# Optimization experiments

Measured on AMD Instinct MI355X. Metric: run time of the kernel, lower is better.

Reference implementation:

```python
import jax, jax.numpy as jnp
import numpy as np

N_NODES = 50000
N_EDGES = 1600000
IN_FEAT = 128
OUT_FEAT = 128
NUM_RELS = 8


def setup_inputs() -> dict:
    key = jax.random.key(0)
    k1, k2, k3, k4, k5, k6, k7 = jax.random.split(key, 7)
    x = jax.random.normal(k1, (N_NODES, IN_FEAT), dtype=jnp.float32)
    norm = jax.random.uniform(k2, (N_EDGES, 1), dtype=jnp.float32)
    src = jax.random.randint(k3, (N_EDGES,), 0, N_NODES)
    dst = jax.random.randint(k4, (N_EDGES,), 0, N_NODES)
    rel_type = jax.random.randint(k5, (N_EDGES,), 0, NUM_RELS)
    # Xavier-uniform-like init for the relation weight tensor (gain for relu)
    gain = float(np.sqrt(2.0))
    bound = gain * float(np.sqrt(6.0 / (IN_FEAT + OUT_FEAT)))
    weight = jax.random.uniform(k6, (NUM_RELS, IN_FEAT, OUT_FEAT), dtype=jnp.float32,
                                minval=-bound, maxval=bound)
    bias = jax.random.uniform(k7, (OUT_FEAT,), dtype=jnp.float32, minval=-0.1, maxval=0.1)
    return {"x": x, "norm": norm, "weight": weight, "bias": bias,
            "src": src, "dst": dst, "rel_type": rel_type}


def reference(x, norm, weight, bias, src, dst, rel_type):
    n_nodes = x.shape[0]
    # Transform every node feature by every relation matrix: [R, N, O].
    # This is equivalent math to the per-edge bmm(h_src, W[rel]) but avoids
    # materializing an [E, in, out] gathered weight tensor.
    hw = jnp.einsum('ni,rio->rno', x, weight)
    # Per-edge message: gather transformed src feature for edge's relation, scale by norm.
    msg = hw[rel_type, src] * norm            # [E, O]
    # Scatter-sum messages to destination nodes.
    h = jax.ops.segment_sum(msg, dst, num_segments=n_nodes)  # [N, O]
    h = jax.nn.relu(h + bias)
    return h
```

## Files before the change

kernel.cpp:

```cpp
#include <hip/hip_runtime.h>
#include <hip/hip_bf16.h>

typedef unsigned short u16;
typedef unsigned int u32;
typedef u16 u16x4 __attribute__((ext_vector_type(4)));
typedef u16 u16x8 __attribute__((ext_vector_type(8)));
typedef short bf16x8 __attribute__((ext_vector_type(8)));
typedef float f32x4 __attribute__((ext_vector_type(4)));

static __device__ __forceinline__ u16 f32_to_bf16(float f) {
    u32 b = __float_as_uint(f);
    u32 r = (b + 0x7fffu + ((b >> 16) & 1u)) >> 16;
    return (u16)r;
}
static __device__ __forceinline__ float bflo(u32 u) { return __uint_as_float(u << 16); }
static __device__ __forceinline__ float bfhi(u32 u) { return __uint_as_float(u & 0xffff0000u); }

static __device__ __forceinline__ void gload_lds16(const void* g, void* l) {
    __builtin_amdgcn_global_load_lds((const __attribute__((address_space(1))) u32*)g,
                                     (__attribute__((address_space(3))) u32*)l, 16, 0, 0);
}

__global__ __launch_bounds__(256) void k_prep(const int* __restrict__ dst, const int* __restrict__ rel,
                                              int* __restrict__ counts, u32* __restrict__ keyrank, int E,
                                              const float* __restrict__ x, u16* __restrict__ xb, int nx,
                                              const float* __restrict__ w, u16* __restrict__ wtb, int nw,
                                              int nbh, int nbx) {
    int bid = blockIdx.x;
    if (bid < nbh) {
        int e = bid * 256 + threadIdx.x;
        if (e < E) {
            int b = dst[e] * 8 + rel[e];
            u32 r = (u32)atomicAdd(&counts[b], 1);
            if (r > 255u) r = 255u;
            keyrank[e] = ((u32)b << 8) | r;
        }
    } else if (bid < nbh + nbx) {
        int i = ((bid - nbh) * 256 + threadIdx.x) * 4;
        if (i < nx) {
            const float4 v = *reinterpret_cast<const float4*>(x + i);
            u16x4 o = { f32_to_bf16(v.x), f32_to_bf16(v.y), f32_to_bf16(v.z), f32_to_bf16(v.w) };
            *reinterpret_cast<u16x4*>(xb + i) = o;
        }
    } else {
        int idx = (bid - nbh - nbx) * 256 + threadIdx.x;
        if (idx < nw) {
            int r = idx >> 14, rem = idx & 16383, o = rem >> 7, i = rem & 127;
            wtb[idx] = f32_to_bf16(w[(r << 14) + (i << 7) + o]);
        }
    }
}

__global__ __launch_bounds__(256) void k_scan1v(const int* __restrict__ counts, int* __restrict__ offsets,
                                                int* __restrict__ bsum, int n) {
    __shared__ int wsum[4];
    int tid = threadIdx.x;
    int base = blockIdx.x * 8192 + tid * 32;
    int4 c[8];
    const int4* cp = reinterpret_cast<const int4*>(counts + base);
#pragma unroll
    for (int j = 0; j < 8; ++j) c[j] = cp[j];
    int t = 0;
#pragma unroll
    for (int j = 0; j < 8; ++j) t += c[j].x + c[j].y + c[j].z + c[j].w;
    int lane = tid & 63, wid = tid >> 6;
    int s = t;
#pragma unroll
    for (int off = 1; off < 64; off <<= 1) {
        int v = __shfl_up(s, off, 64);
        if (lane >= off) s += v;
    }
    if (lane == 63) wsum[wid] = s;
    __syncthreads();
    int woff = 0;
    for (int wq = 0; wq < wid; ++wq) woff += wsum[wq];
    int run = woff + s - t;
    int4* op = reinterpret_cast<int4*>(offsets + base);
#pragma unroll
    for (int j = 0; j < 8; ++j) {
        int4 o;
        o.x = run; run += c[j].x;
        o.y = run; run += c[j].y;
        o.z = run; run += c[j].z;
        o.w = run; run += c[j].w;
        op[j] = o;
    }
    if (tid == 255) bsum[blockIdx.x] = woff + s;
}

__global__ void k_scan2(const int* __restrict__ bsum, int* __restrict__ bo, int* __restrict__ offsets,
                        int nb, int n) {
    int lane = threadIdx.x;
    int v = (lane < nb) ? bsum[lane] : 0;
    int s = v;
#pragma unroll
    for (int off = 1; off < 64; off <<= 1) {
        int u = __shfl_up(s, off, 64);
        if (lane >= off) s += u;
    }
    if (lane < nb) bo[lane] = s - v;
    if (lane == 63) offsets[n] = s;
}

__global__ __launch_bounds__(256) void k_scan3v(int* __restrict__ offsets, const int* __restrict__ bo, int n4) {
    int i = blockIdx.x * 256 + threadIdx.x;
    if (i < n4) {
        int4 v = reinterpret_cast<int4*>(offsets)[i];
        int b = bo[i >> 11];
        v.x += b; v.y += b; v.z += b; v.w += b;
        reinterpret_cast<int4*>(offsets)[i] = v;
    }
}

__global__ __launch_bounds__(256) void k_fill3(const int* __restrict__ src, const float* __restrict__ norm,
                                               const u32* __restrict__ keyrank, const int* __restrict__ offs,
                                               uint2* __restrict__ meta, int E) {
    int e = blockIdx.x * 256 + threadIdx.x;
    if (e < E) {
        u32 kr = keyrank[e];
        int b = (int)(kr >> 8), r = (int)(kr & 255u);
        meta[offs[b] + r] = make_uint2((u32)src[e], __float_as_uint(norm[e]));
    }
}

__global__ __launch_bounds__(256) void k_aggx(const uint2* __restrict__ meta, const int* __restrict__ offs,
                                              const u16* __restrict__ xb, u16* __restrict__ agg,
                                              int M, int E) {
    const int wid4 = __builtin_amdgcn_readfirstlane(threadIdx.x >> 6);
    const int node = blockIdx.x * 4 + wid4;
    if (node >= M) return;
    const int lane4 = (threadIdx.x & 63) << 2;
    const int lane = threadIdx.x & 63;
    const char* xbb = (const char*)xb;
    const int emax = E - 1;
    u32* dstp = reinterpret_cast<u32*>(agg + ((size_t)node << 10));
    int ov[9];
#pragma unroll
    for (int i = 0; i < 9; ++i) ov[i] = offs[node * 8 + i];

#pragma unroll 1
    for (int pass = 0; pass < 2; ++pass) {
        int e[4], en[4];
#pragma unroll
        for (int s = 0; s < 4; ++s) { e[s] = ov[pass * 4 + s]; en[s] = ov[pass * 4 + s + 1]; }
        float a0[4], a1[4], a2[4], a3[4];
#pragma unroll
        for (int s = 0; s < 4; ++s) { a0[s] = 0.f; a1[s] = 0.f; a2[s] = 0.f; a3[s] = 0.f; }

        while (e[0] < en[0] || e[1] < en[1] || e[2] < en[2] || e[3] < en[3]) {
            u32 srow[16], nbits[16];
#pragma unroll
            for (int s = 0; s < 4; ++s)
#pragma unroll
                for (int j = 0; j < 4; ++j) {
                    int ia = e[s] + j;
                    uint2 m = meta[min(ia, emax)];
                    bool ok = ia < en[s];
                    srow[s * 4 + j] = ok ? m.x : 0u;
                    nbits[s * 4 + j] = ok ? m.y : 0u;
                }
            u32 xv[16];
#pragma unroll
            for (int k = 0; k < 16; ++k)
                xv[k] = *(const u32*)(xbb + ((size_t)srow[k] << 8) + lane4);
#pragma unroll
            for (int s = 0; s < 4; ++s) {
#pragma unroll
                for (int j = 0; j < 4; ++j) {
                    float n = __uint_as_float(nbits[s * 4 + j]);
                    u32 v = xv[s * 4 + j];
                    if (j & 1) { a2[s] = fmaf(n, bflo(v), a2[s]); a3[s] = fmaf(n, bfhi(v), a3[s]); }
                    else       { a0[s] = fmaf(n, bflo(v), a0[s]); a1[s] = fmaf(n, bfhi(v), a1[s]); }
                }
                e[s] += 4;
            }
        }
#pragma unroll
        for (int s = 0; s < 4; ++s) {
            u32 pk = (u32)f32_to_bf16(a0[s] + a2[s]) | ((u32)f32_to_bf16(a1[s] + a3[s]) << 16);
            dstp[(pass * 4 + s) * 64 + lane] = pk;
        }
    }
}

__global__ __launch_bounds__(256) void k_gemm2(const u16* __restrict__ agg, const u16* __restrict__ wtb,
                                               const float* __restrict__ bias, float* __restrict__ out, int M) {
    __shared__ u16 As[128 * 128];
    __shared__ u16 Bs[128 * 128];
    const int tid = threadIdx.x;
    const int lane = tid & 63, wid = tid >> 6;
    const int m0 = blockIdx.x * 128;
    const int wm = wid >> 1, wn = wid & 1;
    const int l16 = lane & 15, kg = lane >> 4;
    f32x4 acc[4][4];
#pragma unroll
    for (int a = 0; a < 4; ++a)
#pragma unroll
        for (int b = 0; b < 4; ++b) acc[a][b] = {0.f, 0.f, 0.f, 0.f};

#pragma unroll 1
    for (int g = 0; g < 8; ++g) {
#pragma unroll
        for (int it = 0; it < 8; ++it) {
            int cb = (it * 4 + wid) * 64;
            int c = cb + lane;
            int row = c >> 4;
            int ch = (c & 15) ^ (row & 7);
            int grow = m0 + row;
            if (grow >= M) grow = M - 1;
            gload_lds16(agg + (((size_t)grow << 10) + (g << 7) + (ch << 3)), &As[cb * 8]);
            gload_lds16(wtb + ((g << 14) + (row << 7) + (ch << 3)), &Bs[cb * 8]);
        }
        __syncthreads();
#pragma unroll
        for (int ks = 0; ks < 4; ++ks) {
            const int kb = ks * 32 + kg * 8;
            bf16x8 af[4], bfr[4];
#pragma unroll
            for (int fi = 0; fi < 4; ++fi) {
                int row = wm * 64 + fi * 16 + l16;
                af[fi] = *reinterpret_cast<const bf16x8*>(&As[row * 128 + (kb ^ ((row & 7) << 3))]);
            }
#pragma unroll
            for (int fj = 0; fj < 4; ++fj) {
                int row = wn * 64 + fj * 16 + l16;
                bfr[fj] = *reinterpret_cast<const bf16x8*>(&Bs[row * 128 + (kb ^ ((row & 7) << 3))]);
            }
#pragma unroll
            for (int fi = 0; fi < 4; ++fi)
#pragma unroll
                for (int fj = 0; fj < 4; ++fj)
                    acc[fi][fj] = __builtin_amdgcn_mfma_f32_16x16x32_bf16(af[fi], bfr[fj], acc[fi][fj], 0, 0, 0);
        }
        __syncthreads();
    }
    float bv[4];
#pragma unroll
    for (int fj = 0; fj < 4; ++fj) bv[fj] = bias[wn * 64 + fj * 16 + l16];
#pragma unroll
    for (int fi = 0; fi < 4; ++fi) {
#pragma unroll
        for (int j = 0; j < 4; ++j) {
            int gr = m0 + wm * 64 + fi * 16 + kg * 4 + j;
            if (gr < M) {
                float* rowp = out + (((size_t)gr << 7) + wn * 64 + l16);
#pragma unroll
                for (int fj = 0; fj < 4; ++fj)
                    rowp[fj * 16] = fmaxf(acc[fi][fj][j] + bv[fj], 0.f);
            }
        }
    }
}

extern "C" void kernel_launch(void* const* d_in, const int* in_sizes, int n_in,
                              void* d_out, int out_size, void* d_ws, size_t ws_size,
                              hipStream_t stream) {
    const float* x    = (const float*)d_in[0];
    const float* norm = (const float*)d_in[1];
    const float* w    = (const float*)d_in[2];
    const float* bias = (const float*)d_in[3];
    const int* src    = (const int*)d_in[4];
    const int* dst    = (const int*)d_in[5];
    const int* rel    = (const int*)d_in[6];
    float* out = (float*)d_out;

    const int M = in_sizes[0] / 128;
    const int E = in_sizes[1];
    const int R = 8;
    const int n2 = M * R;
    const int nb = (n2 + 8191) / 8192;
    const int n2p = nb * 8192;

    char* p = (char*)d_ws;
    auto carve = [&p](size_t bytes) -> char* {
        char* r = p;
        p += (bytes + 255) & ~(size_t)255;
        return r;
    };
    u16* xb      = (u16*)carve((size_t)M * 128 * 2);
    u16* wtb     = (u16*)carve((size_t)R * 128 * 128 * 2);
    int* cnt     = (int*)carve((size_t)n2p * 4);
    int* offs    = (int*)carve((size_t)(n2p + 4) * 4);
    int* bsum    = (int*)carve(512);
    int* bo      = (int*)carve(512);
    uint2* meta  = (uint2*)carve((size_t)E * 8);
    u16* agg     = (u16*)carve((size_t)M * 1024 * 2);
    u32* keyrank = (u32*)agg;

    const int nbh = (E + 255) / 256;
    const int nbx = (M * 128 / 4 + 255) / 256;
    const int nbw = (R * 128 * 128 + 255) / 256;

    hipMemsetAsync(cnt, 0, (size_t)n2p * 4, stream);
    k_prep<<<dim3(nbh + nbx + nbw), 256, 0, stream>>>(dst, rel, cnt, keyrank, E,
                                                      x, xb, M * 128, w, wtb, R * 128 * 128,
                                                      nbh, nbx);
    k_scan1v<<<dim3(nb), 256, 0, stream>>>(cnt, offs, bsum, n2p);
    k_scan2<<<dim3(1), 64, 0, stream>>>(bsum, bo, offs, nb, n2p);
    k_scan3v<<<dim3((n2p / 4 + 255) / 256), 256, 0, stream>>>(offs, bo, n2p / 4);
    k_fill3<<<dim3((E + 255) / 256), 256, 0, stream>>>(src, norm, keyrank, offs, meta, E);
    k_aggx<<<dim3((M + 3) / 4), 256, 0, stream>>>(meta, offs, xb, agg, M, E);
    k_gemm2<<<dim3((M + 127) / 128), 256, 0, stream>>>(agg, wtb, bias, out, M);
    (void)ws_size; (void)n_in; (void)out_size;
}
```

Before: 341.8 us.

## Fuse aggregation with relation GEMM and fold block-scan offsets into consumers

Merges the per-node gather-aggregate kernel and the GEMM into one 1024-thread kernel. Sixteen wavefronts each aggregate one node's eight relation rows into LDS, then eight waves multiply that 16-row tile against each relation's weight slice loaded per relation. The second and third scan passes are removed, and each consumer recomputes the block prefix from bsum itself. This drops the global agg round-trip and two launches, at the cost of a small 16-row MFMA tile, weight reloading per 16 nodes, and idle waves during the GEMM phase.

After: 418.8 us. 22.5% more time.

```diff
diff --git a/kernel.cpp b/kernel.cpp
--- a/kernel.cpp
+++ b/kernel.cpp
@@ -88,55 +88,67 @@
     if (tid == 255) bsum[blockIdx.x] = woff + s;
 }
 
-__global__ void k_scan2(const int* __restrict__ bsum, int* __restrict__ bo, int* __restrict__ offsets,
-                        int nb, int n) {
-    int lane = threadIdx.x;
-    int v = (lane < nb) ? bsum[lane] : 0;
-    int s = v;
-#pragma unroll
-    for (int off = 1; off < 64; off <<= 1) {
-        int u = __shfl_up(s, off, 64);
-        if (lane >= off) s += u;
-    }
-    if (lane < nb) bo[lane] = s - v;
-    if (lane == 63) offsets[n] = s;
-}
-
-__global__ __launch_bounds__(256) void k_scan3v(int* __restrict__ offsets, const int* __restrict__ bo, int n4) {
-    int i = blockIdx.x * 256 + threadIdx.x;
-    if (i < n4) {
-        int4 v = reinterpret_cast<int4*>(offsets)[i];
-        int b = bo[i >> 11];
-        v.x += b; v.y += b; v.z += b; v.w += b;
-        reinterpret_cast<int4*>(offsets)[i] = v;
-    }
-}
-
 __global__ __launch_bounds__(256) void k_fill3(const int* __restrict__ src, const float* __restrict__ norm,
-                                               const u32* __restrict__ keyrank, const int* __restrict__ offs,
-                                               uint2* __restrict__ meta, int E) {
-    int e = blockIdx.x * 256 + threadIdx.x;
+                                               const u32* __restrict__ keyrank, const int* __restrict__ offsp,
+                                               const int* __restrict__ bsum, uint2* __restrict__ meta,
+                                               int E, int nbs) {
+    __shared__ int sbo[64];
+    int tid = threadIdx.x;
+    if (tid < 64) {
+        int bval = (tid < nbs) ? bsum[tid] : 0;
+        int s = bval;
+#pragma unroll
+        for (int off = 1; off < 64; off <<= 1) {
+            int v = __shfl_up(s, off, 64);
+            if (tid >= off) s += v;
+        }
+        sbo[tid] = s - bval;
+    }
+    __syncthreads();
+    int e = blockIdx.x * 256 + tid;
     if (e < E) {
         u32 kr = keyrank[e];
         int b = (int)(kr >> 8), r = (int)(kr & 255u);
-        meta[offs[b] + r] = make_uint2((u32)src[e], __float_as_uint(norm[e]));
-    }
-}
-
-__global__ __launch_bounds__(256) void k_aggx(const uint2* __restrict__ meta, const int* __restrict__ offs,
-                                              const u16* __restrict__ xb, u16* __restrict__ agg,
-                                              int M, int E) {
-    const int wid4 = __builtin_amdgcn_readfirstlane(threadIdx.x >> 6);
-    const int node = blockIdx.x * 4 + wid4;
-    if (node >= M) return;
-    const int lane4 = (threadIdx.x & 63) << 2;
-    const int lane = threadIdx.x & 63;
+        meta[offsp[b] + sbo[b >> 13] + r] = make_uint2((u32)src[e], __float_as_uint(norm[e]));
+    }
+}
+
+__global__ __launch_bounds__(1024, 8) void k_fagg(const uint2* __restrict__ meta, const int* __restrict__ offsp,
+                                                  const int* __restrict__ bsum, const u16* __restrict__ xb,
+                                                  const u16* __restrict__ wtb, const float* __restrict__ bias,
+                                                  float* __restrict__ out, int M, int E, int nbs) {
+    __shared__ u16 As[16 * 1024];
+    __shared__ u16 Bs[128 * 128];
+    const int tid = threadIdx.x;
+    const int wu = __builtin_amdgcn_readfirstlane(tid >> 6);
+    const int lane = tid & 63;
+    const int lane4 = lane << 2;
+    const int m0 = blockIdx.x * 16;
+    const int node = m0 + wu;
+    const bool active = node < M;
     const char* xbb = (const char*)xb;
     const int emax = E - 1;
-    u32* dstp = reinterpret_cast<u32*>(agg + ((size_t)node << 10));
+    u32* As32 = reinterpret_cast<u32*>(As);
+
+    int bval = (lane < nbs) ? bsum[lane] : 0;
+    int ssc = bval;
+#pragma unroll
+    for (int off = 1; off < 64; off <<= 1) {
+        int v = __shfl_up(ssc, off, 64);
+        if (lane >= off) ssc += v;
+    }
+    int excl = ssc - bval;
+    const int base = (active ? node : 0) * 8;
+    const int bo0 = __shfl(excl, base >> 13, 64);
+    const int bo1 = __shfl(excl, (base + 8) >> 13, 64);
+
     int ov[9];
 #pragma unroll
-    for (int i = 0; i < 9; ++i) ov[i] = offs[node * 8 + i];
+    for (int i = 0; i < 9; ++i) {
+        int idx = base + i;
+        int bo = ((idx >> 13) == (base >> 13)) ? bo0 : bo1;
+        ov[i] = active ? (offsp[idx] + bo) : 0;
+    }
 
 #pragma unroll 1
     for (int pass = 0; pass < 2; ++pass) {
@@ -177,77 +189,47 @@
         }
 #pragma unroll
         for (int s = 0; s < 4; ++s) {
+            int rr = pass * 4 + s;
             u32 pk = (u32)f32_to_bf16(a0[s] + a2[s]) | ((u32)f32_to_bf16(a1[s] + a3[s]) << 16);
-            dstp[(pass * 4 + s) * 64 + lane] = pk;
-        }
-    }
-}
-
-__global__ __launch_bounds__(256) void k_gemm2(const u16* __restrict__ agg, const u16* __restrict__ wtb,
-                                               const float* __restrict__ bias, float* __restrict__ out, int M) {
-    __shared__ u16 As[128 * 128];
-    __shared__ u16 Bs[128 * 128];
-    const int tid = threadIdx.x;
-    const int lane = tid & 63, wid = tid >> 6;
-    const int m0 = blockIdx.x * 128;
-    const int wm = wid >> 1, wn = wid & 1;
+            int ch = rr * 16 + (lane >> 2);
+            As32[wu * 512 + ((ch ^ (wu & 7)) << 2) + (lane & 3)] = pk;
+        }
+    }
+    __syncthreads();
+
     const int l16 = lane & 15, kg = lane >> 4;
-    f32x4 acc[4][4];
-#pragma unroll
-    for (int a = 0; a < 4; ++a)
-#pragma unroll
-        for (int b = 0; b < 4; ++b) acc[a][b] = {0.f, 0.f, 0.f, 0.f};
-
+    f32x4 acc = {0.f, 0.f, 0.f, 0.f};
 #pragma unroll 1
-    for (int g = 0; g < 8; ++g) {
-#pragma unroll
-        for (int it = 0; it < 8; ++it) {
-            int cb = (it * 4 + wid) * 64;
+    for (int r = 0; r < 8; ++r) {
+#pragma unroll
+        for (int it = 0; it < 2; ++it) {
+            int cb = it * 1024 + wu * 64;
             int c = cb + lane;
             int row = c >> 4;
             int ch = (c & 15) ^ (row & 7);
-            int grow = m0 + row;
-            if (grow >= M) grow = M - 1;
-            gload_lds16(agg + (((size_t)grow << 10) + (g << 7) + (ch << 3)), &As[cb * 8]);
-            gload_lds16(wtb + ((g << 14) + (row << 7) + (ch << 3)), &Bs[cb * 8]);
+            gload_lds16(wtb + ((r << 14) + (row << 7) + (ch << 3)), &Bs[cb * 8]);
         }
         __syncthreads();
-#pragma unroll
-        for (int ks = 0; ks < 4; ++ks) {
-            const int kb = ks * 32 + kg * 8;
-            bf16x8 af[4], bfr[4];
-#pragma unroll
-            for (int fi = 0; fi < 4; ++fi) {
-                int row = wm * 64 + fi * 16 + l16;
-                af[fi] = *reinterpret_cast<const bf16x8*>(&As[row * 128 + (kb ^ ((row & 7) << 3))]);
+        if (wu < 8) {
+#pragma unroll
+            for (int ks = 0; ks < 4; ++ks) {
+                int kb = ks * 32 + kg * 8;
+                int cha = (r * 16 + (kb >> 3)) ^ (l16 & 7);
+                bf16x8 af = *reinterpret_cast<const bf16x8*>(&As[l16 * 1024 + cha * 8]);
+                int brow = wu * 16 + l16;
+                bf16x8 bf = *reinterpret_cast<const bf16x8*>(&Bs[brow * 128 + (kb ^ ((brow & 7) << 3))]);
+                acc = __builtin_amdgcn_mfma_f32_16x16x32_bf16(af, bf, acc, 0, 0, 0);
             }
-#pragma unroll
-            for (int fj = 0; fj < 4; ++fj) {
-                int row = wn * 64 + fj * 16 + l16;
-                bfr[fj] = *reinterpret_cast<const bf16x8*>(&Bs[row * 128 + (kb ^ ((row & 7) << 3))]);
-            }
-#pragma unroll
-            for (int fi = 0; fi < 4; ++fi)
-#pragma unroll
-                for (int fj = 0; fj < 4; ++fj)
-                    acc[fi][fj] = __builtin_amdgcn_mfma_f32_16x16x32_bf16(af[fi], bfr[fj], acc[fi][fj], 0, 0, 0);
         }
         __syncthreads();
     }
-    float bv[4];
-#pragma unroll
-    for (int fj = 0; fj < 4; ++fj) bv[fj] = bias[wn * 64 + fj * 16 + l16];
-#pragma unroll
-    for (int fi = 0; fi < 4; ++fi) {
+    if (wu < 8) {
+        float bv = bias[wu * 16 + l16];
 #pragma unroll
         for (int j = 0; j < 4; ++j) {
-            int gr = m0 + wm * 64 + fi * 16 + kg * 4 + j;
-            if (gr < M) {
-                float* rowp = out + (((size_t)gr << 7) + wn * 64 + l16);
-#pragma unroll
-                for (int fj = 0; fj < 4; ++fj)
-                    rowp[fj * 16] = fmaxf(acc[fi][fj][j] + bv[fj], 0.f);
-            }
+            int gr = m0 + kg * 4 + j;
+            if (gr < M)
+                out[((size_t)gr << 7) + wu * 16 + l16] = fmaxf(acc[j] + bv, 0.f);
         }
     }
 }
@@ -282,10 +264,8 @@
     int* cnt     = (int*)carve((size_t)n2p * 4);
     int* offs    = (int*)carve((size_t)(n2p + 4) * 4);
     int* bsum    = (int*)carve(512);
-    int* bo      = (int*)carve(512);
+    u32* keyrank = (u32*)carve((size_t)E * 4);
     uint2* meta  = (uint2*)carve((size_t)E * 8);
-    u16* agg     = (u16*)carve((size_t)M * 1024 * 2);
-    u32* keyrank = (u32*)agg;
 
     const int nbh = (E + 255) / 256;
     const int nbx = (M * 128 / 4 + 255) / 256;
@@ -296,10 +276,7 @@
                                                       x, xb, M * 128, w, wtb, R * 128 * 128,
                                                       nbh, nbx);
     k_scan1v<<<dim3(nb), 256, 0, stream>>>(cnt, offs, bsum, n2p);
-    k_scan2<<<dim3(1), 64, 0, stream>>>(bsum, bo, offs, nb, n2p);
-    k_scan3v<<<dim3((n2p / 4 + 255) / 256), 256, 0, stream>>>(offs, bo, n2p / 4);
-    k_fill3<<<dim3((E + 255) / 256), 256, 0, stream>>>(src, norm, keyrank, offs, meta, E);
-    k_aggx<<<dim3((M + 3) / 4), 256, 0, stream>>>(meta, offs, xb, agg, M, E);
-    k_gemm2<<<dim3((M + 127) / 128), 256, 0, stream>>>(agg, wtb, bias, out, M);
+    k_fill3<<<dim3((E + 255) / 256), 256, 0, stream>>>(src, norm, keyrank, offs, bsum, meta, E, nb);
+    k_fagg<<<dim3((M + 15) / 16), 1024, 0, stream>>>(meta, offs, bsum, xb, wtb, bias, out, M, E, nb);
     (void)ws_size; (void)n_in; (void)out_size;
 }
```
